# Kernel tuning notes

Measured on AMD Instinct MI355X. Metric: run time of the kernel, lower is better.

The kernel has to match this reference:

```python
import jax, jax.numpy as jnp
import numpy as np

NUM_CLASSES = 345
EPS = 1e-12  # torch F.normalize eps


def setup_inputs() -> dict:
    key = jax.random.key(0)
    k1, k2, k3, k4 = jax.random.split(key, 4)
    B, D, N, C = 65536, 512, 34500, NUM_CLASSES
    z = jax.random.normal(k1, (B, D), dtype=jnp.float32)
    supports = jax.random.normal(k2, (N, D), dtype=jnp.float32)
    ent = jax.random.uniform(k3, (N,), dtype=jnp.float32)
    y_hat = jax.random.randint(k4, (N,), 0, C, dtype=jnp.int32)
    return {"z": z, "supports": supports, "ent": ent, "y_hat": y_hat, "filter_K": 100}


def reference(z, supports, ent, y_hat, filter_K):
    # Per-class top-filter_K selection by lowest entropy, expressed as a mask:
    # globally stable-sort by entropy, then per-class running count via one-hot cumsum.
    C = NUM_CLASSES
    order = jnp.argsort(ent)                      # stable sort -> matches per-class torch.sort tie-break
    y_sorted = y_hat[order]                       # [N]
    onehot = jax.nn.one_hot(y_sorted, C, dtype=z.dtype)  # [N, C]
    # rank (1-based, within own class) of each sorted support
    rank = jnp.sum(jnp.cumsum(onehot, axis=0) * onehot, axis=1)  # [N]
    sel = (rank <= filter_K).astype(z.dtype)      # [N] selection mask

    sup = supports[order]                         # [N, D]
    sup = sup / jnp.maximum(jnp.linalg.norm(sup, axis=1, keepdims=True), EPS)  # row-normalize
    # weights = selected_supports^T @ selected_labels (selection folded into mask)
    weights = jnp.einsum('nd,nc->dc', sup, onehot * sel[:, None])  # [D, C]
    weights = weights / jnp.maximum(jnp.linalg.norm(weights, axis=0, keepdims=True), EPS)
    return z @ weights                            # [B, C]
```

## Files before the change

kernel.cpp:

```cpp
#include <hip/hip_runtime.h>
#include <hip/hip_bf16.h>

#define NCLS 345
#define CPAD 384
#define DIM  512
#define BCAP 256

typedef float f32x4 __attribute__((ext_vector_type(4)));
typedef short s16x8 __attribute__((ext_vector_type(8)));
typedef short s16x4 __attribute__((ext_vector_type(4)));
typedef unsigned long long u64;

__device__ __forceinline__ short f2bf(float f) {
  union { float f; unsigned u; } v; v.f = f;
  unsigned r = v.u + 0x7fffu + ((v.u >> 16) & 1u);
  return (short)(r >> 16);
}

__global__ __launch_bounds__(256) void scan_classes(
    const float* __restrict__ ent, const int* __restrict__ y_hat,
    u64* __restrict__ bucket, int* __restrict__ cnt, int N)
{
  int i = blockIdx.x * 256 + threadIdx.x;
  if (i >= N) return;
  int c = y_hat[i];
  unsigned eb = __float_as_uint(ent[i]);
  u64 key = ((u64)eb << 32) | (unsigned)i;
  int p = atomicAdd(&cnt[c], 1);
  if (p < BCAP) bucket[(size_t)c * BCAP + p] = key;
}

__global__ __launch_bounds__(512) void select_accum(
    const float* __restrict__ supports, const u64* __restrict__ bucket,
    const int* __restrict__ cnt, const int* __restrict__ fKp,
    short* __restrict__ Wp)
{
  const int c = blockIdx.x;
  const int tid = threadIdx.x;
  const int lane = tid & 63, w = tid >> 6;
  __shared__ u64   s_key[BCAP];
  __shared__ int   s_selidx[BCAP];
  __shared__ int   s_nsel;
  __shared__ float s_part[8][DIM];
  __shared__ float s_red[8];
  if (tid == 0) s_nsel = 0;
  const int S = (c < NCLS) ? min(cnt[c], BCAP) : 0;
  const int K = fKp[0];
  for (int e = tid; e < S; e += 512) s_key[e] = bucket[(size_t)c * BCAP + e];
  __syncthreads();
  for (int e = tid; e < S; e += 512) {
    u64 ke = s_key[e];
    int r = 0;
    for (int j = 0; j < S; ++j) r += (s_key[j] < ke) ? 1 : 0;
    if (r < K) { int p = atomicAdd(&s_nsel, 1); s_selidx[p] = (int)(unsigned)(ke & 0xffffffffull); }
  }
  __syncthreads();
  const int nsel = s_nsel;
  f32x4 p0 = {0.f,0.f,0.f,0.f}, p1 = {0.f,0.f,0.f,0.f};
  for (int e0 = w; e0 < nsel; e0 += 16) {
    const int e1 = e0 + 8;
    const bool h1 = (e1 < nsel);
    const f32x4* r0 = (const f32x4*)(supports + (size_t)s_selidx[e0] * DIM);
    f32x4 a0 = r0[lane], a1 = r0[lane + 64];
    f32x4 b0 = {0.f,0.f,0.f,0.f}, b1 = {0.f,0.f,0.f,0.f};
    if (h1) {
      const f32x4* r1 = (const f32x4*)(supports + (size_t)s_selidx[e1] * DIM);
      b0 = r1[lane]; b1 = r1[lane + 64];
    }
    float s0 = 0.f, s1 = 0.f;
#pragma unroll
    for (int j = 0; j < 4; ++j) {
      s0 = fmaf(a0[j], a0[j], s0); s0 = fmaf(a1[j], a1[j], s0);
      s1 = fmaf(b0[j], b0[j], s1); s1 = fmaf(b1[j], b1[j], s1);
    }
#pragma unroll
    for (int off = 32; off; off >>= 1) { s0 += __shfl_xor(s0, off); s1 += __shfl_xor(s1, off); }
    float c0 = 1.f / fmaxf(sqrtf(s0), 1e-12f);
    float c1 = 1.f / fmaxf(sqrtf(s1), 1e-12f);
#pragma unroll
    for (int j = 0; j < 4; ++j) { p0[j] = fmaf(a0[j], c0, p0[j]); p1[j] = fmaf(a1[j], c0, p1[j]); }
    if (h1) {
#pragma unroll
      for (int j = 0; j < 4; ++j) { p0[j] = fmaf(b0[j], c1, p0[j]); p1[j] = fmaf(b1[j], c1, p1[j]); }
    }
  }
  *(f32x4*)&s_part[w][lane * 4]       = p0;
  *(f32x4*)&s_part[w][256 + lane * 4] = p1;
  __syncthreads();
  float acc = 0.f;
#pragma unroll
  for (int ww = 0; ww < 8; ++ww) acc += s_part[ww][tid];
  float sq = acc * acc;
#pragma unroll
  for (int off = 32; off; off >>= 1) sq += __shfl_xor(sq, off);
  if (lane == 0) s_red[w] = sq;
  __syncthreads();
  float tot = 0.f;
#pragma unroll
  for (int ww = 0; ww < 8; ++ww) tot += s_red[ww];
  float sc = 1.f / fmaxf(sqrtf(tot), 1e-12f);
  {
    const int k = tid;
    const int kt = k >> 5, fq = (k >> 3) & 3, j = k & 7;
    const int ct = c >> 4, fr = c & 15;
    const size_t pos = (size_t)(kt * 24 + ct) * 512 + fq * 128 + fr * 8 + j;
    Wp[pos] = f2bf(acc * sc);
  }
}

__global__ __launch_bounds__(512, 4) void gemm_zw(
    const float* __restrict__ z, const short* __restrict__ Wp,
    float* __restrict__ out)
{
  __shared__ __align__(16) char lds[65536];
  const int tid  = threadIdx.x;
  const int lane = tid & 63;
  const int w    = tid >> 6;
  const int fr   = lane & 15, fq = lane >> 4;
  const int Mbase = blockIdx.x * 64;

#pragma unroll
  for (int i = 0; i < 8; ++i) {
    const int row = i * 8 + w;
    const char* src = (const char*)(z + (size_t)(Mbase + row) * DIM);
    f32x4 v0 = *(const f32x4*)(src + lane * 16);
    f32x4 v1 = *(const f32x4*)(src + 1024 + lane * 16);
    s16x4 b0, b1;
#pragma unroll
    for (int j = 0; j < 4; ++j) { b0[j] = f2bf(v0[j]); b1[j] = f2bf(v1[j]); }
    const unsigned so = ((unsigned)(lane >> 1) ^ ((unsigned)row & 7)) * 16 + (lane & 1) * 8;
    *(s16x4*)(lds + row * 1024 + so)       = b0;
    *(s16x4*)(lds + row * 1024 + 512 + so) = b1;
  }
  __syncthreads();

  const char* pb = (const char*)Wp + (size_t)w * 3 * 1024 + (size_t)lane * 16;

  f32x4 acc[4][3];
#pragma unroll
  for (int mt = 0; mt < 4; ++mt)
#pragma unroll
    for (int nt = 0; nt < 3; ++nt) acc[mt][nt] = f32x4{0.f, 0.f, 0.f, 0.f};

  s16x8 Bbuf[4][3];
#pragma unroll
  for (int s = 0; s < 3; ++s)
#pragma unroll
    for (int nt = 0; nt < 3; ++nt)
      Bbuf[s][nt] = *(const s16x8*)(pb + (size_t)s * 24576 + nt * 1024);

#pragma unroll
  for (int t = 0; t < 16; ++t) {
    if (t + 3 < 16) {
#pragma unroll
      for (int nt = 0; nt < 3; ++nt)
        Bbuf[(t + 3) & 3][nt] = *(const s16x8*)(pb + (size_t)(t + 3) * 24576 + nt * 1024);
    }
    s16x8 af[4];
#pragma unroll
    for (int mt = 0; mt < 4; ++mt) {
      const int row = mt * 16 + fr;
      const unsigned slot = ((unsigned)(t * 4) + fq) ^ ((unsigned)row & 7);
      af[mt] = *(const s16x8*)(lds + row * 1024 + slot * 16);
    }
    __builtin_amdgcn_s_setprio(1);
#pragma unroll
    for (int nt = 0; nt < 3; ++nt)
#pragma unroll
      for (int mt = 0; mt < 4; ++mt)
        acc[mt][nt] = __builtin_amdgcn_mfma_f32_16x16x32_bf16(Bbuf[t & 3][nt], af[mt], acc[mt][nt], 0, 0, 0);
    __builtin_amdgcn_s_setprio(0);
  }

#pragma unroll
  for (int h = 0; h < 2; ++h) {
    __syncthreads();
#pragma unroll
    for (int ml = 0; ml < 2; ++ml) {
      const int mt = h * 2 + ml;
      const int rl = ml * 16 + fr;
#pragma unroll
      for (int nt = 0; nt < 3; ++nt) {
        const int colb = w * 48 + nt * 16 + fq * 4;
#pragma unroll
        for (int j = 0; j < 4; ++j) {
          const int col = colb + j;
          if (col < NCLS)
            *(float*)(lds + (((size_t)rl * NCLS + col) << 2)) = acc[mt][nt][j];
        }
      }
    }
    __syncthreads();
    char* dst = (char*)(out + (size_t)(Mbase + h * 32) * NCLS);
    for (int c = tid; c < 2760; c += 512) {
      f32x4 v = *(const f32x4*)(lds + c * 16);
      __builtin_nontemporal_store(v, (f32x4*)(dst + c * 16));
    }
  }
}

extern "C" void kernel_launch(void* const* d_in, const int* in_sizes, int n_in,
                              void* d_out, int out_size, void* d_ws, size_t ws_size,
                              hipStream_t stream) {
  const float* z        = (const float*)d_in[0];
  const float* supports = (const float*)d_in[1];
  const float* ent      = (const float*)d_in[2];
  const int*   y_hat    = (const int*)d_in[3];
  const int*   fK       = (const int*)d_in[4];
  float* out = (float*)d_out;
  short* Wp  = (short*)d_ws;
  const int N = in_sizes[2];
  const int M = in_sizes[0] / DIM;

  const size_t offC = (size_t)CPAD * DIM * 2;
  const size_t offB = offC + 2048;
  int* cnt    = (int*)((char*)d_ws + offC);
  u64* bucket = (u64*)((char*)d_ws + offB);
  hipMemsetAsync(cnt, 0, CPAD * sizeof(int), stream);
  scan_classes<<<dim3((N + 255) / 256), dim3(256), 0, stream>>>(ent, y_hat, bucket, cnt, N);
  select_accum<<<dim3(CPAD), dim3(512), 0, stream>>>(supports, bucket, cnt, fK, Wp);
  gemm_zw<<<dim3(M / 64), dim3(512), 0, stream>>>(z, Wp, out);
}
```

Baseline: 78.28 us.

## Switch z@W GEMM to 32x32x16 MFMA with new LDS and weight layouts

Replaces the 16x16x32 bf16 MFMA tiling (each wave covering all 64 rows and 48 columns) with 32x32x16 MFMA, splitting the waves into two 32-row bands and four 96-column groups. The packed weight layout written by select_accum and the swizzled LDS layout of the bf16 z tile are rewritten to match the new fragment shapes. The epilogue now writes the result to LDS as 16-byte vectors, with a scalar fallback only at the column edge. The aim is fewer MFMA issues and fewer A-fragment LDS reads per FLOP. In exchange it drops the multi-stage register prefetch of B fragments, and the vector LDS stores land at addresses that are not 16-byte aligned because the row stride is 345 floats.

New measurement: 88.26 us. 12.7% more time.

```diff
diff --git a/kernel.cpp b/kernel.cpp
--- a/kernel.cpp
+++ b/kernel.cpp
@@ -6,9 +6,10 @@
 #define DIM  512
 #define BCAP 256
 
-typedef float f32x4 __attribute__((ext_vector_type(4)));
-typedef short s16x8 __attribute__((ext_vector_type(8)));
-typedef short s16x4 __attribute__((ext_vector_type(4)));
+typedef float f32x4  __attribute__((ext_vector_type(4)));
+typedef float f32x16 __attribute__((ext_vector_type(16)));
+typedef short s16x8  __attribute__((ext_vector_type(8)));
+typedef short s16x4  __attribute__((ext_vector_type(4)));
 typedef unsigned long long u64;
 
 __device__ __forceinline__ short f2bf(float f) {
@@ -101,9 +102,10 @@
   float sc = 1.f / fmaxf(sqrtf(tot), 1e-12f);
   {
     const int k = tid;
-    const int kt = k >> 5, fq = (k >> 3) & 3, j = k & 7;
-    const int ct = c >> 4, fr = c & 15;
-    const size_t pos = (size_t)(kt * 24 + ct) * 512 + fq * 128 + fr * 8 + j;
+    const int ct = c >> 5;
+    const int lp = (c & 31) + 32 * ((k >> 3) & 1);
+    const int kt = k >> 4, j = k & 7;
+    const size_t pos = (size_t)(kt * 12 + ct) * 512 + lp * 8 + j;
     Wp[pos] = f2bf(acc * sc);
   }
 }
@@ -116,7 +118,8 @@
   const int tid  = threadIdx.x;
   const int lane = tid & 63;
   const int w    = tid >> 6;
-  const int fr   = lane & 15, fq = lane >> 4;
+  const int band = w >> 2;
+  const int cg   = w & 3;
   const int Mbase = blockIdx.x * 64;
 
 #pragma unroll
@@ -128,65 +131,71 @@
     s16x4 b0, b1;
 #pragma unroll
     for (int j = 0; j < 4; ++j) { b0[j] = f2bf(v0[j]); b1[j] = f2bf(v1[j]); }
-    const unsigned so = ((unsigned)(lane >> 1) ^ ((unsigned)row & 7)) * 16 + (lane & 1) * 8;
-    *(s16x4*)(lds + row * 1024 + so)       = b0;
-    *(s16x4*)(lds + row * 1024 + 512 + so) = b1;
-  }
-  __syncthreads();
-
-  const char* pb = (const char*)Wp + (size_t)w * 3 * 1024 + (size_t)lane * 16;
-
-  f32x4 acc[4][3];
-#pragma unroll
-  for (int mt = 0; mt < 4; ++mt)
-#pragma unroll
-    for (int nt = 0; nt < 3; ++nt) acc[mt][nt] = f32x4{0.f, 0.f, 0.f, 0.f};
-
-  s16x8 Bbuf[4][3];
-#pragma unroll
-  for (int s = 0; s < 3; ++s)
-#pragma unroll
-    for (int nt = 0; nt < 3; ++nt)
-      Bbuf[s][nt] = *(const s16x8*)(pb + (size_t)s * 24576 + nt * 1024);
+    const int rt = row >> 5, r5 = row & 31;
+    const int kt0 = lane >> 2;
+    const int kh  = (lane >> 1) & 1;
+    const int j0  = (lane & 1) * 4;
+    const int slot = (r5 + 32 * kh) ^ (kt0 & 7);
+    char* base = lds + (size_t)rt * 32768 + slot * 16 + j0 * 2;
+    *(s16x4*)(base + kt0 * 1024)        = b0;
+    *(s16x4*)(base + (16 + kt0) * 1024) = b1;
+  }
+  __syncthreads();
+
+  const char* pb = (const char*)Wp + ((size_t)cg * 3) * 1024 + (size_t)lane * 16;
+  const char* pa = lds + (size_t)band * 32768;
+
+  f32x16 acc[3];
+#pragma unroll
+  for (int nt = 0; nt < 3; ++nt)
+#pragma unroll
+    for (int e = 0; e < 16; ++e) acc[nt][e] = 0.f;
 
 #pragma unroll
   for (int t = 0; t < 16; ++t) {
-    if (t + 3 < 16) {
+    s16x8 bf[2][3];
+#pragma unroll
+    for (int kk = 0; kk < 2; ++kk) {
+      const int kt = 2 * t + kk;
 #pragma unroll
       for (int nt = 0; nt < 3; ++nt)
-        Bbuf[(t + 3) & 3][nt] = *(const s16x8*)(pb + (size_t)(t + 3) * 24576 + nt * 1024);
-    }
-    s16x8 af[4];
-#pragma unroll
-    for (int mt = 0; mt < 4; ++mt) {
-      const int row = mt * 16 + fr;
-      const unsigned slot = ((unsigned)(t * 4) + fq) ^ ((unsigned)row & 7);
-      af[mt] = *(const s16x8*)(lds + row * 1024 + slot * 16);
+        bf[kk][nt] = *(const s16x8*)(pb + (size_t)(kt * 12 + nt) * 1024);
+    }
+    s16x8 af[2];
+#pragma unroll
+    for (int kk = 0; kk < 2; ++kk) {
+      const int kt = 2 * t + kk;
+      af[kk] = *(const s16x8*)(pa + kt * 1024 + ((lane ^ (kt & 7)) * 16));
     }
     __builtin_amdgcn_s_setprio(1);
 #pragma unroll
-    for (int nt = 0; nt < 3; ++nt)
-#pragma unroll
-      for (int mt = 0; mt < 4; ++mt)
-        acc[mt][nt] = __builtin_amdgcn_mfma_f32_16x16x32_bf16(Bbuf[t & 3][nt], af[mt], acc[mt][nt], 0, 0, 0);
+    for (int kk = 0; kk < 2; ++kk)
+#pragma unroll
+      for (int nt = 0; nt < 3; ++nt)
+        acc[nt] = __builtin_amdgcn_mfma_f32_32x32x16_bf16(bf[kk][nt], af[kk], acc[nt], 0, 0, 0);
     __builtin_amdgcn_s_setprio(0);
   }
 
+  const int rl = lane & 31;
+  const int half = lane >> 5;
 #pragma unroll
   for (int h = 0; h < 2; ++h) {
     __syncthreads();
-#pragma unroll
-    for (int ml = 0; ml < 2; ++ml) {
-      const int mt = h * 2 + ml;
-      const int rl = ml * 16 + fr;
+    if (band == h) {
 #pragma unroll
       for (int nt = 0; nt < 3; ++nt) {
-        const int colb = w * 48 + nt * 16 + fq * 4;
-#pragma unroll
-        for (int j = 0; j < 4; ++j) {
-          const int col = colb + j;
-          if (col < NCLS)
-            *(float*)(lds + (((size_t)rl * NCLS + col) << 2)) = acc[mt][nt][j];
+#pragma unroll
+        for (int q = 0; q < 4; ++q) {
+          const int col = cg * 96 + nt * 32 + q * 8 + 4 * half;
+          f32x4 v = { acc[nt][q*4], acc[nt][q*4+1], acc[nt][q*4+2], acc[nt][q*4+3] };
+          if (col + 3 < NCLS) {
+            *(f32x4*)(lds + (((size_t)rl * NCLS + col) << 2)) = v;
+          } else if (col < NCLS) {
+#pragma unroll
+            for (int j = 0; j < 4; ++j)
+              if (col + j < NCLS)
+                *(float*)(lds + (((size_t)rl * NCLS + col + j) << 2)) = v[j];
+          }
         }
       }
     }
```
